# Kernel optimization log

Hardware: AMD Instinct MI355X
Metric: run time of the kernel (lower is better)

Reference implementation:

```python
import jax, jax.numpy as jnp
import numpy as np
import math

D_MODEL = 1024
HEADS = 16
D_K = D_MODEL // HEADS
D_FF = 2048
EPS = 1e-6


def layer_norm(x, alpha, bias):
    # torch.std uses unbiased estimator (ddof=1)
    m = x.mean(axis=-1, keepdims=True)
    var = ((x - m) ** 2).sum(axis=-1, keepdims=True) / (x.shape[-1] - 1)
    return alpha * (x - m) / (jnp.sqrt(var) + EPS) + bias


def setup_inputs() -> dict:
    key = jax.random.key(0)
    ks = jax.random.split(key, 12)
    s = 1.0 / math.sqrt(D_MODEL)
    return {
        "x": jax.random.normal(ks[0], (2, 2048, D_MODEL), dtype=jnp.float32),
        "mask": jnp.ones((2, 1, 1, 2048), dtype=jnp.float32),
        "Wq": jax.random.uniform(ks[1], (D_MODEL, D_MODEL), minval=-s, maxval=s),
        "Wk": jax.random.uniform(ks[2], (D_MODEL, D_MODEL), minval=-s, maxval=s),
        "Wv": jax.random.uniform(ks[3], (D_MODEL, D_MODEL), minval=-s, maxval=s),
        "Wo": jax.random.uniform(ks[4], (D_MODEL, D_MODEL), minval=-s, maxval=s),
        "bo": jnp.zeros((D_MODEL,), dtype=jnp.float32),
        "W1": jax.random.uniform(ks[5], (D_MODEL, D_FF), minval=-s, maxval=s),
        "b1": jnp.zeros((D_FF,), dtype=jnp.float32),
        "W2": jax.random.uniform(ks[6], (D_FF, D_MODEL), minval=-1.0 / math.sqrt(D_FF), maxval=1.0 / math.sqrt(D_FF)),
        "b2": jnp.zeros((D_MODEL,), dtype=jnp.float32),
        "ln1_a": jnp.ones((D_MODEL,), dtype=jnp.float32),
        "ln1_b": jnp.zeros((D_MODEL,), dtype=jnp.float32),
        "ln2_a": jnp.ones((D_MODEL,), dtype=jnp.float32),
        "ln2_b": jnp.zeros((D_MODEL,), dtype=jnp.float32),
    }


def reference(x, mask, Wq, Wk, Wv, Wo, bo, W1, b1, W2, b2, ln1_a, ln1_b, ln2_a, ln2_b):
    B, S, _ = x.shape
    # --- attention sublayer (pre-LN) ---
    x2 = layer_norm(x, ln1_a, ln1_b)
    q = (x2 @ Wq).reshape(B, S, HEADS, D_K).transpose(0, 2, 1, 3)  # [B,H,S,dk]
    k = (x2 @ Wk).reshape(B, S, HEADS, D_K).transpose(0, 2, 1, 3)
    v = (x2 @ Wv).reshape(B, S, HEADS, D_K).transpose(0, 2, 1, 3)
    attn = jnp.einsum("bhqd,bhkd->bhqk", q, k) / math.sqrt(D_K)
    attn = attn * mask                                  # multiplicative mask
    attn = jnp.where(attn == 0.0, -jnp.inf, attn)       # masked_fill(==0, -inf)
    scores = jax.nn.softmax(attn, axis=-1)
    av = jnp.einsum("bhqk,bhkd->bhqd", scores, v)
    concat = av.transpose(0, 2, 1, 3).reshape(B, S, D_MODEL)
    x = x + (concat @ Wo + bo)
    # --- FFN sublayer (pre-LN) ---
    x2 = layer_norm(x, ln2_a, ln2_b)
    h = jax.nn.relu(x2 @ W1 + b1)
    x = x + (h @ W2 + b2)
    return x
```

## Files before the change

kernel.cpp:

```cpp
#include <hip/hip_runtime.h>
#include <hip/hip_bf16.h>

typedef unsigned short u16;
typedef __attribute__((ext_vector_type(4))) float f32x4;
typedef __attribute__((ext_vector_type(8))) short bf16x8;

#define SEQ 2048
#define DM 1024
#define DKK 64
#define NH 16
#define DFF 2048
#define TOK 4096

#define AS1 __attribute__((address_space(1)))
#define AS3 __attribute__((address_space(3)))

#define MFMA16(a, b, c) __builtin_amdgcn_mfma_f32_16x16x32_bf16((a), (b), (c), 0, 0, 0)

__device__ __forceinline__ u16 f2b(float f) {
  unsigned u = __float_as_uint(f);
  u = u + 0x7fffu + ((u >> 16) & 1u);
  return (u16)(u >> 16);
}

__device__ __forceinline__ unsigned cvtpk(float lo, float hi) {
  unsigned r;
  asm("v_cvt_pk_bf16_f32 %0, %1, %2" : "=v"(r) : "v"(lo), "v"(hi));
  return r;
}

__device__ __forceinline__ void gload_lds16(const u16* g, u16* l) {
  __builtin_amdgcn_global_load_lds((AS1 unsigned*)(size_t)g, (AS3 unsigned*)l, 16, 0, 0);
}

__global__ __launch_bounds__(256)
void prep_all(const float* __restrict__ Wq, const float* __restrict__ Wk,
              const float* __restrict__ Wv, const float* __restrict__ Wo,
              const float* __restrict__ W1, const float* __restrict__ W2,
              u16* __restrict__ Wqkt, u16* __restrict__ Wvt, u16* __restrict__ Wot,
              u16* __restrict__ W1t, u16* __restrict__ W2t,
              const float* __restrict__ x, const float* __restrict__ alpha,
              const float* __restrict__ beta, u16* __restrict__ xout) {
  __shared__ float t[32][33];
  const int bid = blockIdx.x;
  const int tid = threadIdx.x;
  if (bid < 8192) {
    const float* src;
    u16* dst;
    int K, N, lb;
    if (bid < 1024)      { src = Wq; dst = Wqkt;             K = 1024; N = 1024; lb = bid; }
    else if (bid < 2048) { src = Wk; dst = Wqkt + (1 << 20); K = 1024; N = 1024; lb = bid - 1024; }
    else if (bid < 3072) { src = Wv; dst = Wvt;              K = 1024; N = 1024; lb = bid - 2048; }
    else if (bid < 4096) { src = Wo; dst = Wot;              K = 1024; N = 1024; lb = bid - 3072; }
    else if (bid < 6144) { src = W1; dst = W1t;              K = 1024; N = 2048; lb = bid - 4096; }
    else                 { src = W2; dst = W2t;              K = 2048; N = 1024; lb = bid - 6144; }
    const int nx = N / 32;
    const int n0 = (lb % nx) * 32, k0 = (lb / nx) * 32;
    const int tx = tid & 31, ty = tid >> 5;
#pragma unroll
    for (int i = 0; i < 4; i++) {
      int k = ty + i * 8;
      t[k][tx] = src[(size_t)(k0 + k) * N + n0 + tx];
    }
    __syncthreads();
#pragma unroll
    for (int i = 0; i < 4; i++) {
      int n = ty + i * 8;
      dst[(size_t)(n0 + n) * K + k0 + tx] = f2b(t[tx][n]);
    }
  } else {
    const int row = bid - 8192;
    const float4 v = ((const float4*)(x + (size_t)row * DM))[tid];
    float s = v.x + v.y + v.z + v.w;
    float q = v.x * v.x + v.y * v.y + v.z * v.z + v.w * v.w;
#pragma unroll
    for (int off = 1; off < 64; off <<= 1) {
      s += __shfl_xor(s, off);
      q += __shfl_xor(q, off);
    }
    float* ss = &t[0][0];
    float* qq = &t[0][8];
    const int wid = tid >> 6;
    if ((tid & 63) == 0) { ss[wid] = s; qq[wid] = q; }
    __syncthreads();
    s = ss[0] + ss[1] + ss[2] + ss[3];
    q = qq[0] + qq[1] + qq[2] + qq[3];
    const float mean = s * (1.f / DM);
    float var = (q - (float)DM * mean * mean) * (1.f / (DM - 1));
    var = fmaxf(var, 0.f);
    const float inv = 1.f / (sqrtf(var) + 1e-6f);
    const float4 a4 = ((const float4*)alpha)[tid];
    const float4 b4 = ((const float4*)beta)[tid];
    ushort4 o;
    o.x = f2b((v.x - mean) * inv * a4.x + b4.x);
    o.y = f2b((v.y - mean) * inv * a4.y + b4.y);
    o.z = f2b((v.z - mean) * inv * a4.z + b4.z);
    o.w = f2b((v.w - mean) * inv * a4.w + b4.w);
    ((ushort4*)(xout + (size_t)row * DM))[tid] = o;
  }
}

__global__ __launch_bounds__(256)
void ln_kernel(const float* __restrict__ x, const float* __restrict__ alpha,
               const float* __restrict__ beta, u16* __restrict__ out) {
  const int row = blockIdx.x;
  const float4 v = ((const float4*)(x + (size_t)row * DM))[threadIdx.x];
  float s = v.x + v.y + v.z + v.w;
  float q = v.x * v.x + v.y * v.y + v.z * v.z + v.w * v.w;
#pragma unroll
  for (int off = 1; off < 64; off <<= 1) {
    s += __shfl_xor(s, off);
    q += __shfl_xor(q, off);
  }
  __shared__ float ss[4], qq[4];
  const int wid = threadIdx.x >> 6;
  if ((threadIdx.x & 63) == 0) { ss[wid] = s; qq[wid] = q; }
  __syncthreads();
  s = ss[0] + ss[1] + ss[2] + ss[3];
  q = qq[0] + qq[1] + qq[2] + qq[3];
  const float mean = s * (1.f / DM);
  float var = (q - (float)DM * mean * mean) * (1.f / (DM - 1));
  var = fmaxf(var, 0.f);
  const float inv = 1.f / (sqrtf(var) + 1e-6f);
  const float4 a4 = ((const float4*)alpha)[threadIdx.x];
  const float4 b4 = ((const float4*)beta)[threadIdx.x];
  ushort4 o;
  o.x = f2b((v.x - mean) * inv * a4.x + b4.x);
  o.y = f2b((v.y - mean) * inv * a4.y + b4.y);
  o.z = f2b((v.z - mean) * inv * a4.z + b4.z);
  o.w = f2b((v.w - mean) * inv * a4.w + b4.w);
  ((ushort4*)(out + (size_t)row * DM))[threadIdx.x] = o;
}

__global__ __launch_bounds__(256, 4)
void qkv_gemm(const u16* __restrict__ x2, const u16* __restrict__ Wqkt,
              const u16* __restrict__ Wvt,
              u16* __restrict__ qkb, u16* __restrict__ vtb, float oscale) {
  constexpr int BM = 64, BN = 128, AccM = 2, AccN = 4;
  __shared__ alignas(16) u16 As[3][BM * 32];
  __shared__ alignas(16) u16 Bs[3][BN * 32];
  const int bid = blockIdx.x;
  const int K = DM;
  const u16* A;
  const u16* Bt;
  int bm, bn, mode;
  if (bid < 1024) {
    mode = 0; A = x2; Bt = Wqkt;
    bm = (bid & 63) * BM; bn = (bid >> 6) * BN;
  } else {
    mode = 1; A = Wvt; Bt = x2;
    const int lb = bid - 1024;
    bm = (lb & 15) * BM; bn = (lb >> 4) * BN;
  }
  const int tid = threadIdx.x;
  const int lane = tid & 63, w = tid >> 6;
  const int wm = (w >> 1) * (BM / 2), wn = (w & 1) * (BN / 2);
  const int r = lane & 15, g = lane >> 4;
  const int srow = tid >> 2, skk = (tid & 3) * 8;

  f32x4 acc[AccM][AccN];
#pragma unroll
  for (int i = 0; i < AccM; i++)
#pragma unroll
    for (int j = 0; j < AccN; j++) acc[i][j] = (f32x4){0.f, 0.f, 0.f, 0.f};

  const u16* aP = A + (size_t)(bm + srow) * K + skk;
  const u16* bP = Bt + (size_t)(bn + srow) * K + skk;

  auto stage = [&](int kt, int buf) {
    gload_lds16(aP + kt, &As[buf][0] + w * 512);
    gload_lds16(bP + kt, &Bs[buf][0] + w * 512);
    gload_lds16(bP + (size_t)64 * K + kt, &Bs[buf][0] + w * 512 + 2048);
  };
  auto waitL = [&]() { asm volatile("s_waitcnt vmcnt(3) lgkmcnt(0)" ::: "memory"); };
  auto compute = [&](int buf) {
    bf16x8 af[AccM], bfr[AccN];
#pragma unroll
    for (int i = 0; i < AccM; i++) af[i] = *(const bf16x8*)(&As[buf][(wm + i * 16 + r) * 32 + g * 8]);
#pragma unroll
    for (int j = 0; j < AccN; j++) bfr[j] = *(const bf16x8*)(&Bs[buf][(wn + j * 16 + r) * 32 + g * 8]);
#pragma unroll
    for (int i = 0; i < AccM; i++)
#pragma unroll
      for (int j = 0; j < AccN; j++) acc[i][j] = MFMA16(af[i], bfr[j], acc[i][j]);
  };

  const int NKT = K / 32;
  stage(0, 0);
  stage(32, 1);
  waitL();
  __builtin_amdgcn_s_barrier();
  __builtin_amdgcn_sched_barrier(0);
  for (int it = 0; it < NKT - 2; ++it) {
    stage((it + 2) * 32, (it + 2) % 3);
    compute(it % 3);
    waitL();
    __builtin_amdgcn_s_barrier();
    __builtin_amdgcn_sched_barrier(0);
  }
  compute((NKT - 2) % 3);
  asm volatile("s_waitcnt vmcnt(0) lgkmcnt(0)" ::: "memory");
  __builtin_amdgcn_s_barrier();
  __builtin_amdgcn_sched_barrier(0);
  compute((NKT - 1) % 3);

#pragma unroll
  for (int i = 0; i < AccM; i++)
#pragma unroll
    for (int j = 0; j < AccN; j++)
#pragma unroll
      for (int t = 0; t < 4; t++) {
        const int mg = bm + wm + i * 16 + g * 4 + t;
        const int ng = bn + wn + j * 16 + r;
        const float v = acc[i][j][t];
        if (mode == 0) {
          const int which = ng >> 10, col = ng & 1023;
          const int bb = mg >> 11, ssx = mg & 2047, hh = col >> 6, dd = col & 63;
          const float sc = which ? 1.f : oscale;
          qkb[(size_t)which * (TOK * (size_t)DM) +
              ((size_t)(bb * NH + hh) * SEQ + ssx) * DKK + dd] = f2b(v * sc);
        } else {
          const int hh = mg >> 6, dd = mg & 63, bb = ng >> 11, ssx = ng & 2047;
          vtb[((size_t)(bb * NH + hh) * DKK + dd) * SEQ + ssx] = f2b(v);
        }
      }
}

template <int MODE, int BM, int BN>
__global__ __launch_bounds__(256, 4)
void gemm_bt(const u16* __restrict__ A, const u16* __restrict__ Bt,
             int M, int N, int K,
             const float* __restrict__ bias, const float* __restrict__ res,
             void* __restrict__ outp) {
  constexpr int AccM = BM / 32;
  constexpr int AccN = BN / 32;
  constexpr int L = (BM == 128 ? 2 : 1) + (BN == 128 ? 2 : 1);
  __shared__ alignas(16) u16 As[3][BM * 32];
  __shared__ alignas(16) u16 Bs[3][BN * 32];
  const int bm = blockIdx.x * BM, bn = blockIdx.y * BN;
  const int tid = threadIdx.x;
  const int lane = tid & 63, w = tid >> 6;
  const int wm = (w >> 1) * (BM / 2), wn = (w & 1) * (BN / 2);
  const int r = lane & 15, g = lane >> 4;
  const int srow = tid >> 2, skk = (tid & 3) * 8;

  f32x4 acc[AccM][AccN];
#pragma unroll
  for (int i = 0; i < AccM; i++)
#pragma unroll
    for (int j = 0; j < AccN; j++) acc[i][j] = (f32x4){0.f, 0.f, 0.f, 0.f};

  const u16* aP = A + (size_t)(bm + srow) * K + skk;
  const u16* bP = Bt + (size_t)(bn + srow) * K + skk;

  auto stage = [&](int kt, int buf) {
    gload_lds16(aP + kt, &As[buf][0] + w * 512);
    if (BM == 128) gload_lds16(aP + (size_t)64 * K + kt, &As[buf][0] + w * 512 + 2048);
    gload_lds16(bP + kt, &Bs[buf][0] + w * 512);
    if (BN == 128) gload_lds16(bP + (size_t)64 * K + kt, &Bs[buf][0] + w * 512 + 2048);
  };
  auto waitL = [&]() {
    if constexpr (L == 4) asm volatile("s_waitcnt vmcnt(4) lgkmcnt(0)" ::: "memory");
    else if constexpr (L == 3) asm volatile("s_waitcnt vmcnt(3) lgkmcnt(0)" ::: "memory");
    else asm volatile("s_waitcnt vmcnt(2) lgkmcnt(0)" ::: "memory");
  };
  auto compute = [&](int buf) {
    bf16x8 af[AccM], bfr[AccN];
#pragma unroll
    for (int i = 0; i < AccM; i++) af[i] = *(const bf16x8*)(&As[buf][(wm + i * 16 + r) * 32 + g * 8]);
#pragma unroll
    for (int j = 0; j < AccN; j++) bfr[j] = *(const bf16x8*)(&Bs[buf][(wn + j * 16 + r) * 32 + g * 8]);
#pragma unroll
    for (int i = 0; i < AccM; i++)
#pragma unroll
      for (int j = 0; j < AccN; j++) acc[i][j] = MFMA16(af[i], bfr[j], acc[i][j]);
  };

  const int NKT = K / 32;
  stage(0, 0);
  stage(32, 1);
  waitL();
  __builtin_amdgcn_s_barrier();
  __builtin_amdgcn_sched_barrier(0);
  for (int it = 0; it < NKT - 2; ++it) {
    stage((it + 2) * 32, (it + 2) % 3);
    compute(it % 3);
    waitL();
    __builtin_amdgcn_s_barrier();
    __builtin_amdgcn_sched_barrier(0);
  }
  compute((NKT - 2) % 3);
  asm volatile("s_waitcnt vmcnt(0) lgkmcnt(0)" ::: "memory");
  __builtin_amdgcn_s_barrier();
  __builtin_amdgcn_sched_barrier(0);
  compute((NKT - 1) % 3);

#pragma unroll
  for (int i = 0; i < AccM; i++)
#pragma unroll
    for (int j = 0; j < AccN; j++)
#pragma unroll
      for (int t = 0; t < 4; t++) {
        const int mg = bm + wm + i * 16 + g * 4 + t;
        const int ng = bn + wn + j * 16 + r;
        const float v = acc[i][j][t];
        if (MODE == 2) {
          ((float*)outp)[(size_t)mg * N + ng] = res[(size_t)mg * N + ng] + v + bias[ng];
        } else {
          const float hv = v + bias[ng];
          ((u16*)outp)[(size_t)mg * N + ng] = f2b(hv > 0.f ? hv : 0.f);
        }
      }
}

__global__ __launch_bounds__(256, 4)
void attn_kernel(const u16* __restrict__ Q, const u16* __restrict__ Kb,
                 const u16* __restrict__ Vt, const float* __restrict__ mask,
                 u16* __restrict__ outc) {
  const int bid = blockIdx.x;
  const int bh = (bid & 7) * 4 + ((bid >> 3) & 3);
  const int qt = bid >> 5;
  const int b = bh >> 4, h = bh & 15;
  const int tid = threadIdx.x, lane = tid & 63, w = tid >> 6;
  const int r = lane & 15, g = lane >> 4;
  const int qbase = qt * 64 + w * 16;
  const u16* Qp = Q + ((size_t)bh * SEQ + qbase) * DKK;
  const u16* Kp = Kb + (size_t)bh * SEQ * DKK;
  const u16* Vp = Vt + (size_t)bh * DKK * SEQ;
  const float* mk = mask + b * SEQ;

  const bf16x8 bq0 = *(const bf16x8*)(Qp + r * DKK + g * 8);
  const bf16x8 bq1 = *(const bf16x8*)(Qp + r * DKK + 32 + g * 8);

  __shared__ __align__(16) u16 Ks[2][64 * 64];
  __shared__ __align__(16) u16 Vs[2][64 * 64];

  const int srow8 = lane >> 3;
  const int sgr = (lane & 7) ^ srow8;
  const u16* kSrc1 = Kp + (size_t)(w * 16 + srow8) * DKK + sgr * 8;
  const u16* kSrc2 = kSrc1 + 8 * DKK;
  const u16* vSrc1 = Vp + (size_t)(w * 16 + srow8) * SEQ + sgr * 8;
  const u16* vSrc2 = vSrc1 + 8 * SEQ;

  f32x4 o[4];
#pragma unroll
  for (int i = 0; i < 4; i++) o[i] = (f32x4){0.f, 0.f, 0.f, 0.f};
  float lr = 0.f;
  const int keyr = r & 7;

  gload_lds16(kSrc1, &Ks[0][0] + w * 1024);
  gload_lds16(kSrc2, &Ks[0][0] + w * 1024 + 512);
  gload_lds16(vSrc1, &Vs[0][0] + w * 1024);
  gload_lds16(vSrc2, &Vs[0][0] + w * 1024 + 512);
  asm volatile("s_waitcnt vmcnt(0)" ::: "memory");
  __builtin_amdgcn_s_barrier();
  __builtin_amdgcn_sched_barrier(0);

  const int NT = SEQ / 64;

#define ATTN_STEP(IT, BUF)                                                         \
  do {                                                                             \
    if ((IT) + 1 < NT) {                                                           \
      const int nsk = ((IT) + 1) * 64;                                             \
      u16* kd = &Ks[(BUF) ^ 1][0] + w * 1024;                                      \
      gload_lds16(kSrc1 + (size_t)nsk * DKK, kd);                                  \
      gload_lds16(kSrc2 + (size_t)nsk * DKK, kd + 512);                            \
      u16* vd = &Vs[(BUF) ^ 1][0] + w * 1024;                                      \
      gload_lds16(vSrc1 + nsk, vd);                                                \
      gload_lds16(vSrc2 + nsk, vd + 512);                                          \
    }                                                                              \
    f32x4 s[4];                                                                    \
    __builtin_amdgcn_s_setprio(1);                                                 \
    _Pragma("unroll")                                                              \
    for (int ks = 0; ks < 4; ks++) {                                               \
      const bf16x8 ka0 = *(const bf16x8*)&Ks[BUF][(ks * 16 + r) * 64 + ((g ^ keyr) << 3)];        \
      const bf16x8 ka1 = *(const bf16x8*)&Ks[BUF][(ks * 16 + r) * 64 + (((g + 4) ^ keyr) << 3)];  \
      f32x4 z = (f32x4){0.f, 0.f, 0.f, 0.f};                                       \
      z = MFMA16(ka0, bq0, z);                                                     \
      z = MFMA16(ka1, bq1, z);                                                     \
      s[ks] = z;                                                                   \
    }                                                                              \
    __builtin_amdgcn_s_setprio(0);                                                 \
    const int sk = (IT) * 64;                                                      \
    float4 mmv[4];                                                                 \
    _Pragma("unroll")                                                              \
    for (int ks = 0; ks < 4; ks++) mmv[ks] = *(const float4*)(mk + sk + ks * 16 + 4 * g); \
    int ones = 1;                                                                  \
    _Pragma("unroll")                                                              \
    for (int ks = 0; ks < 4; ks++)                                                 \
      ones &= (mmv[ks].x == 1.f) & (mmv[ks].y == 1.f) & (mmv[ks].z == 1.f) & (mmv[ks].w == 1.f); \
    const bool fastm = __all(ones);                                                \
    float p[16];                                                                   \
    float rs = 0.f;                                                                \
    if (fastm) {                                                                   \
      _Pragma("unroll")                                                            \
      for (int ks = 0; ks < 4; ks++) {                                             \
        float e0 = __builtin_amdgcn_exp2f(s[ks][0]);                               \
        float e1 = __builtin_amdgcn_exp2f(s[ks][1]);                               \
        float e2 = __builtin_amdgcn_exp2f(s[ks][2]);                               \
        float e3 = __builtin_amdgcn_exp2f(s[ks][3]);                               \
        p[ks * 4 + 0] = e0; p[ks * 4 + 1] = e1;                                    \
        p[ks * 4 + 2] = e2; p[ks * 4 + 3] = e3;                                    \
        rs += e0 + e1 + e2 + e3;                                                   \
      }                                                                            \
    } else {                                                                       \
      _Pragma("unroll")                                                            \
      for (int ks = 0; ks < 4; ks++) {                                             \
        float pr0 = s[ks][0] * mmv[ks].x, pr1 = s[ks][1] * mmv[ks].y;              \
        float pr2 = s[ks][2] * mmv[ks].z, pr3 = s[ks][3] * mmv[ks].w;              \
        float e0 = (pr0 == 0.f) ? 0.f : __builtin_amdgcn_exp2f(pr0);               \
        float e1 = (pr1 == 0.f) ? 0.f : __builtin_amdgcn_exp2f(pr1);               \
        float e2 = (pr2 == 0.f) ? 0.f : __builtin_amdgcn_exp2f(pr2);               \
        float e3 = (pr3 == 0.f) ? 0.f : __builtin_amdgcn_exp2f(pr3);               \
        p[ks * 4 + 0] = e0; p[ks * 4 + 1] = e1;                                    \
        p[ks * 4 + 2] = e2; p[ks * 4 + 3] = e3;                                    \
        rs += e0 + e1 + e2 + e3;                                                   \
      }                                                                            \
    }                                                                              \
    rs += __shfl_xor(rs, 16);                                                      \
    rs += __shfl_xor(rs, 32);                                                      \
    lr += rs;                                                                      \
    unsigned wk[4][2];                                                             \
    _Pragma("unroll")                                                              \
    for (int ks = 0; ks < 4; ks++) {                                               \
      wk[ks][0] = cvtpk(p[ks * 4 + 0], p[ks * 4 + 1]);                             \
      wk[ks][1] = cvtpk(p[ks * 4 + 2], p[ks * 4 + 3]);                             \
    }                                                                              \
    bf16x8 pa[2];                                                                  \
    _Pragma("unroll")                                                              \
    for (int hh2 = 0; hh2 < 2; hh2++) {                                            \
      union { unsigned u[4]; bf16x8 v; } pu;                                       \
      _Pragma("unroll")                                                            \
      for (int c = 0; c < 4; c++) {                                                \
        const int srcl = r + ((g & 1) * 2 + (c >> 1)) * 16;                        \
        const unsigned lo = __shfl(wk[2 * hh2][c & 1], srcl);                      \
        const unsigned hi = __shfl(wk[2 * hh2 + 1][c & 1], srcl);                  \
        pu.u[c] = (g < 2) ? lo : hi;                                               \
      }                                                                            \
      pa[hh2] = pu.v;                                                              \
    }                                                                              \
    __builtin_amdgcn_s_setprio(1);                                                 \
    _Pragma("unroll")                                                              \
    for (int dc = 0; dc < 4; dc++) {                                               \
      const int vr = dc * 16 + r;                                                  \
      const bf16x8 bv0 = *(const bf16x8*)&Vs[BUF][vr * 64 + ((g ^ keyr) << 3)];    \
      const bf16x8 bv1 = *(const bf16x8*)&Vs[BUF][vr * 64 + (((g + 4) ^ keyr) << 3)]; \
      o[dc] = MFMA16(pa[0], bv0, o[dc]);                                           \
      o[dc] = MFMA16(pa[1], bv1, o[dc]);                                           \
    }                                                                              \
    __builtin_amdgcn_s_setprio(0);                                                 \
    asm volatile("s_waitcnt vmcnt(0) lgkmcnt(0)" ::: "memory");                    \
    __builtin_amdgcn_s_barrier();                                                  \
    __builtin_amdgcn_sched_barrier(0);                                             \
  } while (0)

  for (int it = 0; it < NT; it += 2) {
    ATTN_STEP(it, 0);
    ATTN_STEP(it + 1, 1);
  }
#undef ATTN_STEP

  float lq[4];
#pragma unroll
  for (int t = 0; t < 4; t++) lq[t] = __shfl(lr, 4 * g + t);
#pragma unroll
  for (int dc = 0; dc < 4; dc++)
#pragma unroll
    for (int t = 0; t < 4; t++) {
      const int srow_g = qbase + g * 4 + t;
      outc[((size_t)(b * SEQ + srow_g)) * DM + h * DKK + dc * 16 + r] = f2b(o[dc][t] / lq[t]);
    }
}

extern "C" void kernel_launch(void* const* d_in, const int* in_sizes, int n_in,
                              void* d_out, int out_size, void* d_ws, size_t ws_size,
                              hipStream_t stream) {
  const float* x    = (const float*)d_in[0];
  const float* mask = (const float*)d_in[1];
  const float* Wq   = (const float*)d_in[2];
  const float* Wk   = (const float*)d_in[3];
  const float* Wv   = (const float*)d_in[4];
  const float* Wo   = (const float*)d_in[5];
  const float* bo   = (const float*)d_in[6];
  const float* W1   = (const float*)d_in[7];
  const float* b1   = (const float*)d_in[8];
  const float* W2   = (const float*)d_in[9];
  const float* b2   = (const float*)d_in[10];
  const float* l1a  = (const float*)d_in[11];
  const float* l1b  = (const float*)d_in[12];
  const float* l2a  = (const float*)d_in[13];
  const float* l2b  = (const float*)d_in[14];

  char* wsb = (char*)d_ws;
  u16* Wqkt = (u16*)(wsb + (0ull << 20));
  u16* Wvt  = (u16*)(wsb + (4ull << 20));
  u16* Wot  = (u16*)(wsb + (6ull << 20));
  u16* W1t  = (u16*)(wsb + (8ull << 20));
  u16* W2t  = (u16*)(wsb + (12ull << 20));
  u16* x2   = (u16*)(wsb + (16ull << 20));
  u16* qkb  = (u16*)(wsb + (24ull << 20));
  u16* vtb  = (u16*)(wsb + (40ull << 20));
  float* x1 = (float*)(wsb + (48ull << 20));
  u16* concat = x2;
  u16* x2b = qkb;
  u16* hb  = (u16*)(wsb + (32ull << 20));

  const float qscale = 0.125f * 1.4426950408889634f;

  prep_all<<<dim3(12288), 256, 0, stream>>>(Wq, Wk, Wv, Wo, W1, W2,
                                            Wqkt, Wvt, Wot, W1t, W2t,
                                            x, l1a, l1b, x2);

  qkv_gemm<<<dim3(1536), 256, 0, stream>>>(x2, Wqkt, Wvt, qkb, vtb, qscale);

  attn_kernel<<<dim3(1024), 256, 0, stream>>>(qkb, qkb + (size_t)TOK * DM, vtb, mask, concat);

  gemm_bt<2, 64, 64><<<dim3(TOK / 64, DM / 64), 256, 0, stream>>>(
      concat, Wot, TOK, DM, DM, bo, x, x1);

  ln_kernel<<<TOK, 256, 0, stream>>>(x1, l2a, l2b, x2b);

  gemm_bt<3, 64, 128><<<dim3(TOK / 64, DFF / 128), 256, 0, stream>>>(
      x2b, W1t, TOK, DFF, DM, b1, nullptr, hb);
  gemm_bt<2, 64, 64><<<dim3(TOK / 64, DM / 64), 256, 0, stream>>>(
      hb, W2t, TOK, DM, DFF, b2, x1, (float*)d_out);
}
```

Measured before the change: 218.9 us.

## Software-pipeline attention loop: overlap QK^T of next tile with softmax/PV of previous

Restructures the attention key loop so that each iteration computes QK^T scores for tile t while doing the exp/softmax and PV MFMAs for tile t-1. V gets a triple buffer and K stays double-buffered, with the buffers rotated through pointer swaps, and an epilogue handles the last tile. The goal is to interleave independent MFMA and exp/VALU work and hide latency. In exchange it uses more LDS and registers and turns the unrolled-by-two loop into pointer-based indexing, which may affect occupancy and address computation.

Result: no change. 221.0 us (+1.0%).

```diff
diff --git a/kernel.cpp b/kernel.cpp
--- a/kernel.cpp
+++ b/kernel.cpp
@@ -333,7 +333,7 @@
   const bf16x8 bq1 = *(const bf16x8*)(Qp + r * DKK + 32 + g * 8);
 
   __shared__ __align__(16) u16 Ks[2][64 * 64];
-  __shared__ __align__(16) u16 Vs[2][64 * 64];
+  __shared__ __align__(16) u16 Vs[3][64 * 64];
 
   const int srow8 = lane >> 3;
   const int sgr = (lane & 7) ^ srow8;
@@ -348,117 +348,192 @@
   float lr = 0.f;
   const int keyr = r & 7;
 
-  gload_lds16(kSrc1, &Ks[0][0] + w * 1024);
-  gload_lds16(kSrc2, &Ks[0][0] + w * 1024 + 512);
-  gload_lds16(vSrc1, &Vs[0][0] + w * 1024);
-  gload_lds16(vSrc2, &Vs[0][0] + w * 1024 + 512);
+  u16* kCur = &Ks[0][0];
+  u16* kNxt = &Ks[1][0];
+  u16* vComp = &Vs[2][0];
+  u16* vReady = &Vs[0][0];
+  u16* vStage = &Vs[1][0];
+
+  gload_lds16(kSrc1, kCur + w * 1024);
+  gload_lds16(kSrc2, kCur + w * 1024 + 512);
+  gload_lds16(vSrc1, vReady + w * 1024);
+  gload_lds16(vSrc2, vReady + w * 1024 + 512);
   asm volatile("s_waitcnt vmcnt(0)" ::: "memory");
   __builtin_amdgcn_s_barrier();
   __builtin_amdgcn_sched_barrier(0);
 
+  f32x4 s[4];
+#pragma unroll
+  for (int i = 0; i < 4; i++) s[i] = (f32x4){0.f, 0.f, 0.f, 0.f};
+
   const int NT = SEQ / 64;
-
-#define ATTN_STEP(IT, BUF)                                                         \
-  do {                                                                             \
-    if ((IT) + 1 < NT) {                                                           \
-      const int nsk = ((IT) + 1) * 64;                                             \
-      u16* kd = &Ks[(BUF) ^ 1][0] + w * 1024;                                      \
-      gload_lds16(kSrc1 + (size_t)nsk * DKK, kd);                                  \
-      gload_lds16(kSrc2 + (size_t)nsk * DKK, kd + 512);                            \
-      u16* vd = &Vs[(BUF) ^ 1][0] + w * 1024;                                      \
-      gload_lds16(vSrc1 + nsk, vd);                                                \
-      gload_lds16(vSrc2 + nsk, vd + 512);                                          \
-    }                                                                              \
-    f32x4 s[4];                                                                    \
-    __builtin_amdgcn_s_setprio(1);                                                 \
-    _Pragma("unroll")                                                              \
-    for (int ks = 0; ks < 4; ks++) {                                               \
-      const bf16x8 ka0 = *(const bf16x8*)&Ks[BUF][(ks * 16 + r) * 64 + ((g ^ keyr) << 3)];        \
-      const bf16x8 ka1 = *(const bf16x8*)&Ks[BUF][(ks * 16 + r) * 64 + (((g + 4) ^ keyr) << 3)];  \
-      f32x4 z = (f32x4){0.f, 0.f, 0.f, 0.f};                                       \
-      z = MFMA16(ka0, bq0, z);                                                     \
-      z = MFMA16(ka1, bq1, z);                                                     \
-      s[ks] = z;                                                                   \
-    }                                                                              \
-    __builtin_amdgcn_s_setprio(0);                                                 \
-    const int sk = (IT) * 64;                                                      \
-    float4 mmv[4];                                                                 \
-    _Pragma("unroll")                                                              \
-    for (int ks = 0; ks < 4; ks++) mmv[ks] = *(const float4*)(mk + sk + ks * 16 + 4 * g); \
-    int ones = 1;                                                                  \
-    _Pragma("unroll")                                                              \
-    for (int ks = 0; ks < 4; ks++)                                                 \
-      ones &= (mmv[ks].x == 1.f) & (mmv[ks].y == 1.f) & (mmv[ks].z == 1.f) & (mmv[ks].w == 1.f); \
-    const bool fastm = __all(ones);                                                \
-    float p[16];                                                                   \
-    float rs = 0.f;                                                                \
-    if (fastm) {                                                                   \
-      _Pragma("unroll")                                                            \
-      for (int ks = 0; ks < 4; ks++) {                                             \
-        float e0 = __builtin_amdgcn_exp2f(s[ks][0]);                               \
-        float e1 = __builtin_amdgcn_exp2f(s[ks][1]);                               \
-        float e2 = __builtin_amdgcn_exp2f(s[ks][2]);                               \
-        float e3 = __builtin_amdgcn_exp2f(s[ks][3]);                               \
-        p[ks * 4 + 0] = e0; p[ks * 4 + 1] = e1;                                    \
-        p[ks * 4 + 2] = e2; p[ks * 4 + 3] = e3;                                    \
-        rs += e0 + e1 + e2 + e3;                                                   \
-      }                                                                            \
-    } else {                                                                       \
-      _Pragma("unroll")                                                            \
-      for (int ks = 0; ks < 4; ks++) {                                             \
-        float pr0 = s[ks][0] * mmv[ks].x, pr1 = s[ks][1] * mmv[ks].y;              \
-        float pr2 = s[ks][2] * mmv[ks].z, pr3 = s[ks][3] * mmv[ks].w;              \
-        float e0 = (pr0 == 0.f) ? 0.f : __builtin_amdgcn_exp2f(pr0);               \
-        float e1 = (pr1 == 0.f) ? 0.f : __builtin_amdgcn_exp2f(pr1);               \
-        float e2 = (pr2 == 0.f) ? 0.f : __builtin_amdgcn_exp2f(pr2);               \
-        float e3 = (pr3 == 0.f) ? 0.f : __builtin_amdgcn_exp2f(pr3);               \
-        p[ks * 4 + 0] = e0; p[ks * 4 + 1] = e1;                                    \
-        p[ks * 4 + 2] = e2; p[ks * 4 + 3] = e3;                                    \
-        rs += e0 + e1 + e2 + e3;                                                   \
-      }                                                                            \
-    }                                                                              \
-    rs += __shfl_xor(rs, 16);                                                      \
-    rs += __shfl_xor(rs, 32);                                                      \
-    lr += rs;                                                                      \
-    unsigned wk[4][2];                                                             \
-    _Pragma("unroll")                                                              \
-    for (int ks = 0; ks < 4; ks++) {                                               \
-      wk[ks][0] = cvtpk(p[ks * 4 + 0], p[ks * 4 + 1]);                             \
-      wk[ks][1] = cvtpk(p[ks * 4 + 2], p[ks * 4 + 3]);                             \
-    }                                                                              \
-    bf16x8 pa[2];                                                                  \
-    _Pragma("unroll")                                                              \
-    for (int hh2 = 0; hh2 < 2; hh2++) {                                            \
-      union { unsigned u[4]; bf16x8 v; } pu;                                       \
-      _Pragma("unroll")                                                            \
-      for (int c = 0; c < 4; c++) {                                                \
-        const int srcl = r + ((g & 1) * 2 + (c >> 1)) * 16;                        \
-        const unsigned lo = __shfl(wk[2 * hh2][c & 1], srcl);                      \
-        const unsigned hi = __shfl(wk[2 * hh2 + 1][c & 1], srcl);                  \
-        pu.u[c] = (g < 2) ? lo : hi;                                               \
-      }                                                                            \
-      pa[hh2] = pu.v;                                                              \
-    }                                                                              \
-    __builtin_amdgcn_s_setprio(1);                                                 \
-    _Pragma("unroll")                                                              \
-    for (int dc = 0; dc < 4; dc++) {                                               \
-      const int vr = dc * 16 + r;                                                  \
-      const bf16x8 bv0 = *(const bf16x8*)&Vs[BUF][vr * 64 + ((g ^ keyr) << 3)];    \
-      const bf16x8 bv1 = *(const bf16x8*)&Vs[BUF][vr * 64 + (((g + 4) ^ keyr) << 3)]; \
-      o[dc] = MFMA16(pa[0], bv0, o[dc]);                                           \
-      o[dc] = MFMA16(pa[1], bv1, o[dc]);                                           \
-    }                                                                              \
-    __builtin_amdgcn_s_setprio(0);                                                 \
-    asm volatile("s_waitcnt vmcnt(0) lgkmcnt(0)" ::: "memory");                    \
-    __builtin_amdgcn_s_barrier();                                                  \
-    __builtin_amdgcn_sched_barrier(0);                                             \
-  } while (0)
-
-  for (int it = 0; it < NT; it += 2) {
-    ATTN_STEP(it, 0);
-    ATTN_STEP(it + 1, 1);
+  for (int t = 0; t < NT; ++t) {
+    if (t + 1 < NT) {
+      const int nsk = (t + 1) * 64;
+      gload_lds16(kSrc1 + (size_t)nsk * DKK, kNxt + w * 1024);
+      gload_lds16(kSrc2 + (size_t)nsk * DKK, kNxt + w * 1024 + 512);
+      gload_lds16(vSrc1 + nsk, vStage + w * 1024);
+      gload_lds16(vSrc2 + nsk, vStage + w * 1024 + 512);
+    }
+    f32x4 sn[4];
+    __builtin_amdgcn_s_setprio(1);
+#pragma unroll
+    for (int ks = 0; ks < 4; ks++) {
+      const bf16x8 ka0 = *(const bf16x8*)(kCur + (ks * 16 + r) * 64 + ((g ^ keyr) << 3));
+      const bf16x8 ka1 = *(const bf16x8*)(kCur + (ks * 16 + r) * 64 + (((g + 4) ^ keyr) << 3));
+      f32x4 z = (f32x4){0.f, 0.f, 0.f, 0.f};
+      z = MFMA16(ka0, bq0, z);
+      z = MFMA16(ka1, bq1, z);
+      sn[ks] = z;
+    }
+    __builtin_amdgcn_s_setprio(0);
+    if (t > 0) {
+      const int skp = (t - 1) * 64;
+      float4 mmv[4];
+#pragma unroll
+      for (int ks = 0; ks < 4; ks++) mmv[ks] = *(const float4*)(mk + skp + ks * 16 + 4 * g);
+      int ones = 1;
+#pragma unroll
+      for (int ks = 0; ks < 4; ks++)
+        ones &= (mmv[ks].x == 1.f) & (mmv[ks].y == 1.f) & (mmv[ks].z == 1.f) & (mmv[ks].w == 1.f);
+      const bool fastm = __all(ones);
+      float p[16];
+      float rs = 0.f;
+      if (fastm) {
+#pragma unroll
+        for (int ks = 0; ks < 4; ks++) {
+          float e0 = __builtin_amdgcn_exp2f(s[ks][0]);
+          float e1 = __builtin_amdgcn_exp2f(s[ks][1]);
+          float e2 = __builtin_amdgcn_exp2f(s[ks][2]);
+          float e3 = __builtin_amdgcn_exp2f(s[ks][3]);
+          p[ks * 4 + 0] = e0; p[ks * 4 + 1] = e1;
+          p[ks * 4 + 2] = e2; p[ks * 4 + 3] = e3;
+          rs += e0 + e1 + e2 + e3;
+        }
+      } else {
+#pragma unroll
+        for (int ks = 0; ks < 4; ks++) {
+          float pr0 = s[ks][0] * mmv[ks].x, pr1 = s[ks][1] * mmv[ks].y;
+          float pr2 = s[ks][2] * mmv[ks].z, pr3 = s[ks][3] * mmv[ks].w;
+          float e0 = (pr0 == 0.f) ? 0.f : __builtin_amdgcn_exp2f(pr0);
+          float e1 = (pr1 == 0.f) ? 0.f : __builtin_amdgcn_exp2f(pr1);
+          float e2 = (pr2 == 0.f) ? 0.f : __builtin_amdgcn_exp2f(pr2);
+          float e3 = (pr3 == 0.f) ? 0.f : __builtin_amdgcn_exp2f(pr3);
+          p[ks * 4 + 0] = e0; p[ks * 4 + 1] = e1;
+          p[ks * 4 + 2] = e2; p[ks * 4 + 3] = e3;
+          rs += e0 + e1 + e2 + e3;
+        }
+      }
+      rs += __shfl_xor(rs, 16);
+      rs += __shfl_xor(rs, 32);
+      lr += rs;
+      unsigned wk[4][2];
+#pragma unroll
+      for (int ks = 0; ks < 4; ks++) {
+        wk[ks][0] = cvtpk(p[ks * 4 + 0], p[ks * 4 + 1]);
+        wk[ks][1] = cvtpk(p[ks * 4 + 2], p[ks * 4 + 3]);
+      }
+      bf16x8 pa[2];
+#pragma unroll
+      for (int hh2 = 0; hh2 < 2; hh2++) {
+        union { unsigned u[4]; bf16x8 v; } pu;
+#pragma unroll
+        for (int c = 0; c < 4; c++) {
+          const int srcl = r + ((g & 1) * 2 + (c >> 1)) * 16;
+          const unsigned lo = __shfl(wk[2 * hh2][c & 1], srcl);
+          const unsigned hi = __shfl(wk[2 * hh2 + 1][c & 1], srcl);
+          pu.u[c] = (g < 2) ? lo : hi;
+        }
+        pa[hh2] = pu.v;
+      }
+      __builtin_amdgcn_s_setprio(1);
+#pragma unroll
+      for (int dc = 0; dc < 4; dc++) {
+        const int vr = dc * 16 + r;
+        const bf16x8 bv0 = *(const bf16x8*)(vComp + vr * 64 + ((g ^ keyr) << 3));
+        const bf16x8 bv1 = *(const bf16x8*)(vComp + vr * 64 + (((g + 4) ^ keyr) << 3));
+        o[dc] = MFMA16(pa[0], bv0, o[dc]);
+        o[dc] = MFMA16(pa[1], bv1, o[dc]);
+      }
+      __builtin_amdgcn_s_setprio(0);
+    }
+#pragma unroll
+    for (int i = 0; i < 4; i++) s[i] = sn[i];
+    u16* tv = vComp; vComp = vReady; vReady = vStage; vStage = tv;
+    u16* tk = kCur; kCur = kNxt; kNxt = tk;
+    asm volatile("s_waitcnt vmcnt(0) lgkmcnt(0)" ::: "memory");
+    __builtin_amdgcn_s_barrier();
+    __builtin_amdgcn_sched_barrier(0);
   }
-#undef ATTN_STEP
+
+  {
+    const int skp = (NT - 1) * 64;
+    float4 mmv[4];
+#pragma unroll
+    for (int ks = 0; ks < 4; ks++) mmv[ks] = *(const float4*)(mk + skp + ks * 16 + 4 * g);
+    int ones = 1;
+#pragma unroll
+    for (int ks = 0; ks < 4; ks++)
+      ones &= (mmv[ks].x == 1.f) & (mmv[ks].y == 1.f) & (mmv[ks].z == 1.f) & (mmv[ks].w == 1.f);
+    const bool fastm = __all(ones);
+    float p[16];
+    float rs = 0.f;
+    if (fastm) {
+#pragma unroll
+      for (int ks = 0; ks < 4; ks++) {
+        float e0 = __builtin_amdgcn_exp2f(s[ks][0]);
+        float e1 = __builtin_amdgcn_exp2f(s[ks][1]);
+        float e2 = __builtin_amdgcn_exp2f(s[ks][2]);
+        float e3 = __builtin_amdgcn_exp2f(s[ks][3]);
+        p[ks * 4 + 0] = e0; p[ks * 4 + 1] = e1;
+        p[ks * 4 + 2] = e2; p[ks * 4 + 3] = e3;
+        rs += e0 + e1 + e2 + e3;
+      }
+    } else {
+#pragma unroll
+      for (int ks = 0; ks < 4; ks++) {
+        float pr0 = s[ks][0] * mmv[ks].x, pr1 = s[ks][1] * mmv[ks].y;
+        float pr2 = s[ks][2] * mmv[ks].z, pr3 = s[ks][3] * mmv[ks].w;
+        float e0 = (pr0 == 0.f) ? 0.f : __builtin_amdgcn_exp2f(pr0);
+        float e1 = (pr1 == 0.f) ? 0.f : __builtin_amdgcn_exp2f(pr1);
+        float e2 = (pr2 == 0.f) ? 0.f : __builtin_amdgcn_exp2f(pr2);
+        float e3 = (pr3 == 0.f) ? 0.f : __builtin_amdgcn_exp2f(pr3);
+        p[ks * 4 + 0] = e0; p[ks * 4 + 1] = e1;
+        p[ks * 4 + 2] = e2; p[ks * 4 + 3] = e3;
+        rs += e0 + e1 + e2 + e3;
+      }
+    }
+    rs += __shfl_xor(rs, 16);
+    rs += __shfl_xor(rs, 32);
+    lr += rs;
+    unsigned wk[4][2];
+#pragma unroll
+    for (int ks = 0; ks < 4; ks++) {
+      wk[ks][0] = cvtpk(p[ks * 4 + 0], p[ks * 4 + 1]);
+      wk[ks][1] = cvtpk(p[ks * 4 + 2], p[ks * 4 + 3]);
+    }
+    bf16x8 pa[2];
+#pragma unroll
+    for (int hh2 = 0; hh2 < 2; hh2++) {
+      union { unsigned u[4]; bf16x8 v; } pu;
+#pragma unroll
+      for (int c = 0; c < 4; c++) {
+        const int srcl = r + ((g & 1) * 2 + (c >> 1)) * 16;
+        const unsigned lo = __shfl(wk[2 * hh2][c & 1], srcl);
+        const unsigned hi = __shfl(wk[2 * hh2 + 1][c & 1], srcl);
+        pu.u[c] = (g < 2) ? lo : hi;
+      }
+      pa[hh2] = pu.v;
+    }
+#pragma unroll
+    for (int dc = 0; dc < 4; dc++) {
+      const int vr = dc * 16 + r;
+      const bf16x8 bv0 = *(const bf16x8*)(vComp + vr * 64 + ((g ^ keyr) << 3));
+      const bf16x8 bv1 = *(const bf16x8*)(vComp + vr * 64 + (((g + 4) ^ keyr) << 3));
+      o[dc] = MFMA16(pa[0], bv0, o[dc]);
+      o[dc] = MFMA16(pa[1], bv1, o[dc]);
+    }
+  }
 
   float lq[4];
 #pragma unroll
```
